# Kernel optimization log

Measured on AMD Instinct MI355X. Metric: run time of the kernel, lower is better.

Reference implementation:

```python
import jax, jax.numpy as jnp
import numpy as np

N = 50000   # nodes
E = 800000  # directed edges
D = 128     # input_feat_dim
H = 128     # hidden1
L = 3       # GatedGraphConv layers
G = 64      # num graphs in batch
NEG_SLOPE = 0.01


def setup_inputs() -> dict:
    key = jax.random.key(0)
    ks = jax.random.split(key, 12)
    s = 1.0 / np.sqrt(H)
    x = jax.random.normal(ks[0], (N, D), jnp.float32)
    edge_index = jax.random.randint(ks[1], (2, E), 0, N)
    batch = jnp.sort(jax.random.randint(ks[2], (N,), 0, G))
    W_gcn = jax.random.normal(ks[3], (D, H), jnp.float32) * s
    b_gcn = jnp.zeros((H,), jnp.float32)
    W_gg = jax.random.normal(ks[4], (L, H, H), jnp.float32) * s   # GatedGraphConv per-layer weight
    W_ih = jax.random.normal(ks[5], (3 * H, H), jnp.float32) * s  # GRUCell input weights (r,z,n)
    W_hh = jax.random.normal(ks[6], (3 * H, H), jnp.float32) * s  # GRUCell hidden weights
    b_ih = jnp.zeros((3 * H,), jnp.float32)
    b_hh = jnp.zeros((3 * H,), jnp.float32)
    W1 = jax.random.normal(ks[7], (H, H), jnp.float32) * s
    b1 = jnp.zeros((H,), jnp.float32)
    W2 = jax.random.normal(ks[8], (H, 1), jnp.float32) * s
    b2 = jnp.zeros((1,), jnp.float32)
    return dict(x=x, edge_index=edge_index, batch=batch, W_gcn=W_gcn, b_gcn=b_gcn,
                W_gg=W_gg, W_ih=W_ih, W_hh=W_hh, b_ih=b_ih, b_hh=b_hh,
                W1=W1, b1=b1, W2=W2, b2=b2)


def _seg(vals, idx, num):
    return jax.ops.segment_sum(vals, idx, num_segments=num)


def _gcn(x, row, col, W, b):
    # PyG GCNConv: add self loops, symmetric norm, aggregate at target (col)
    xw = x @ W
    deg = _seg(jnp.ones((E,), xw.dtype), col, N) + 1.0  # +1 for self loop
    dinv = jax.lax.rsqrt(deg)
    norm = dinv[row] * dinv[col]                         # [E]
    out = _seg(xw[row] * norm[:, None], col, N)          # gather-scale-scatter
    out = out + xw * (dinv * dinv)[:, None]              # self-loop term
    return out + b


def _gru(m, h, W_ih, W_hh, b_ih, b_hh):
    gi = m @ W_ih.T + b_ih
    gh = h @ W_hh.T + b_hh
    ir, iz, inn = jnp.split(gi, 3, axis=-1)
    hr, hz, hn = jnp.split(gh, 3, axis=-1)
    r = jax.nn.sigmoid(ir + hr)
    z = jax.nn.sigmoid(iz + hz)
    n = jnp.tanh(inn + r * hn)
    return (1.0 - z) * n + z * h


def reference(x, edge_index, batch, W_gcn, b_gcn, W_gg, W_ih, W_hh, b_ih, b_hh, W1, b1, W2, b2):
    row, col = edge_index[0], edge_index[1]
    h = jax.nn.leaky_relu(_gcn(x, row, col, W_gcn, b_gcn), NEG_SLOPE)   # [N,H]
    g = h
    for l in range(L):  # GatedGraphConv: message = x_j @ W_l, sum-aggregate at col, GRU update
        m = _seg((g @ W_gg[l])[row], col, N)
        g = _gru(m, g, W_ih, W_hh, b_ih, b_hh)
    h = jax.nn.leaky_relu(g, NEG_SLOPE) + h
    h = jax.nn.leaky_relu(h @ W1 + b1, NEG_SLOPE)
    probs = jax.nn.sigmoid(h @ W2 + b2)                                  # [N,1]
    # maxcut loss: per-graph expected cut
    degrees = _seg(jnp.ones((E,), probs.dtype), row, N)[:, None]         # degree(row) per node
    expected_weight = _seg(probs[row] * probs[col], batch[row], G)       # [G,1]
    expected_degree = _seg(probs * degrees, batch, G)                    # [G,1]
    return -(expected_degree - expected_weight) / 2.0                    # [G,1]
```

## Files before the change

kernel.cpp:

```cpp
#include <hip/hip_runtime.h>
#include <math.h>

#define HD 128
#define NEG 0.01f
#define GD 64
#define LDST 136
#define FST 132

typedef short bf16x8 __attribute__((ext_vector_type(8)));
typedef float floatx4 __attribute__((ext_vector_type(4)));

__device__ __forceinline__ unsigned short f2bf(float f) {
    unsigned int u = __float_as_uint(f);
    u += 0x7fffu + ((u >> 16) & 1u);
    return (unsigned short)(u >> 16);
}
__device__ __forceinline__ float bf2f(unsigned short b) {
    return __uint_as_float(((unsigned int)b) << 16);
}
__device__ __forceinline__ float sigm(float v) { return 1.f / (1.f + __expf(-v)); }

__device__ __forceinline__ void mm64(const unsigned short* __restrict__ ap,
                                     const unsigned short* __restrict__ W,
                                     int m16, int quad, floatx4* acc) {
    #pragma unroll
    for (int ks = 0; ks < 4; ks++) {
        const int koff = ks * 32 + quad * 8;
        bf16x8 a = *(const bf16x8*)(ap + koff);
        #pragma unroll
        for (int cg = 0; cg < 8; cg++) {
            bf16x8 b = *(const bf16x8*)(W + (size_t)(cg * 16 + m16) * HD + koff);
            acc[cg] = __builtin_amdgcn_mfma_f32_16x16x32_bf16(a, b, acc[cg], 0, 0, 0);
        }
    }
}

__device__ __forceinline__ void loadB(const unsigned short* __restrict__ W,
                                      int w, int m16, int quad, bf16x8 bf[2][4]) {
    #pragma unroll
    for (int cgl = 0; cgl < 2; cgl++)
        #pragma unroll
        for (int ks = 0; ks < 4; ks++)
            bf[cgl][ks] = *(const bf16x8*)(W + (size_t)((2 * w + cgl) * 16 + m16) * HD
                                           + ks * 32 + quad * 8);
}
__device__ __forceinline__ void mmAcc32(const unsigned short* __restrict__ Atile,
                                        int m16, int quad, const bf16x8 bf[2][4],
                                        floatx4 acc[2][2]) {
    #pragma unroll
    for (int rg = 0; rg < 2; rg++)
        #pragma unroll
        for (int ks = 0; ks < 4; ks++) {
            bf16x8 a = *(const bf16x8*)(Atile + (rg * 16 + m16) * LDST + ks * 32 + quad * 8);
            acc[rg][0] = __builtin_amdgcn_mfma_f32_16x16x32_bf16(a, bf[0][ks], acc[rg][0], 0, 0, 0);
            acc[rg][1] = __builtin_amdgcn_mfma_f32_16x16x32_bf16(a, bf[1][ks], acc[rg][1], 0, 0, 0);
        }
}

__global__ __launch_bounds__(256) void gemm_mfma(
    const unsigned short* __restrict__ A, const unsigned short* __restrict__ BT,
    float* __restrict__ C32, unsigned short* __restrict__ C16, int M)
{
    __shared__ unsigned short As[128 * LDST];
    __shared__ unsigned short Bs[128 * LDST];
    const int tid = threadIdx.x;
    const int r0 = blockIdx.x * 128;
    {
        int rowi = tid >> 1, half = tid & 1;
        int gr = r0 + rowi; if (gr >= M) gr = M - 1;
        const float4* sa = (const float4*)(A + (size_t)gr * HD + half * 64);
        float4* da = (float4*)(As + rowi * LDST + half * 64);
        const float4* sb = (const float4*)(BT + (size_t)rowi * HD + half * 64);
        float4* db = (float4*)(Bs + rowi * LDST + half * 64);
        #pragma unroll
        for (int i = 0; i < 8; i++) { da[i] = sa[i]; db[i] = sb[i]; }
    }
    __syncthreads();
    const int wave = tid >> 6, lane = tid & 63;
    const int m16 = lane & 15, quad = lane >> 4;
    floatx4 acc[2][8];
    #pragma unroll
    for (int i = 0; i < 2; i++)
        #pragma unroll
        for (int j = 0; j < 8; j++) acc[i][j] = (floatx4){0.f, 0.f, 0.f, 0.f};
    const unsigned short* ar0 = As + (wave * 32 + m16) * LDST;
    const unsigned short* ar1 = As + (wave * 32 + 16 + m16) * LDST;
    #pragma unroll
    for (int ks = 0; ks < 4; ks++) {
        const int koff = ks * 32 + quad * 8;
        bf16x8 a0 = *(const bf16x8*)(ar0 + koff);
        bf16x8 a1 = *(const bf16x8*)(ar1 + koff);
        #pragma unroll
        for (int cg = 0; cg < 8; cg++) {
            bf16x8 b = *(const bf16x8*)(Bs + (cg * 16 + m16) * LDST + koff);
            acc[0][cg] = __builtin_amdgcn_mfma_f32_16x16x32_bf16(a0, b, acc[0][cg], 0, 0, 0);
            acc[1][cg] = __builtin_amdgcn_mfma_f32_16x16x32_bf16(a1, b, acc[1][cg], 0, 0, 0);
        }
    }
    if (C32) {
        #pragma unroll
        for (int rg = 0; rg < 2; rg++)
            #pragma unroll
            for (int cg = 0; cg < 8; cg++)
                #pragma unroll
                for (int i = 0; i < 4; i++) {
                    int r = r0 + wave * 32 + rg * 16 + quad * 4 + i;
                    if (r < M) C32[(size_t)r * HD + cg * 16 + m16] = acc[rg][cg][i];
                }
    }
    __syncthreads();
    #pragma unroll
    for (int rg = 0; rg < 2; rg++)
        #pragma unroll
        for (int cg = 0; cg < 8; cg++)
            #pragma unroll
            for (int i = 0; i < 4; i++)
                As[(wave * 32 + rg * 16 + quad * 4 + i) * LDST + cg * 16 + m16] =
                    f2bf(acc[rg][cg][i]);
    __syncthreads();
    #pragma unroll
    for (int it = 0; it < 8; it++) {
        int idx = it * 2048 + tid * 8;
        int rowi = idx >> 7, c = idx & 127;
        int gr = r0 + rowi;
        if (gr < M) {
            uint4 v = *(const uint4*)(As + rowi * LDST + c);
            *(uint4*)(C16 + (size_t)gr * HD + c) = v;
        }
    }
}

__global__ __launch_bounds__(256) void k_gather_gcn(
    const unsigned short* __restrict__ src, const float* __restrict__ xw,
    const int* __restrict__ csr, const int* __restrict__ offs,
    const float* __restrict__ dinv, const float* __restrict__ bias,
    float* __restrict__ h, unsigned short* __restrict__ g16, int N)
{
    int node = blockIdx.x * 4 + (threadIdx.x >> 6);
    if (node >= N) return;
    int lane = threadIdx.x & 63;
    int s = offs[node], e = offs[node + 1];
    float ax = 0.f, ay = 0.f;
    int j = s;
    for (; j + 4 <= e; j += 4) {
        int r0 = csr[j], r1 = csr[j + 1], r2 = csr[j + 2], r3 = csr[j + 3];
        unsigned int u0 = *(const unsigned int*)(src + (size_t)r0 * HD + lane * 2);
        unsigned int u1 = *(const unsigned int*)(src + (size_t)r1 * HD + lane * 2);
        unsigned int u2 = *(const unsigned int*)(src + (size_t)r2 * HD + lane * 2);
        unsigned int u3 = *(const unsigned int*)(src + (size_t)r3 * HD + lane * 2);
        float s0 = dinv[r0], s1 = dinv[r1], s2 = dinv[r2], s3 = dinv[r3];
        ax += __uint_as_float(u0 << 16) * s0 + __uint_as_float(u1 << 16) * s1
            + __uint_as_float(u2 << 16) * s2 + __uint_as_float(u3 << 16) * s3;
        ay += __uint_as_float(u0 & 0xffff0000u) * s0 + __uint_as_float(u1 & 0xffff0000u) * s1
            + __uint_as_float(u2 & 0xffff0000u) * s2 + __uint_as_float(u3 & 0xffff0000u) * s3;
    }
    for (; j < e; j++) {
        int r = csr[j];
        unsigned int u = *(const unsigned int*)(src + (size_t)r * HD + lane * 2);
        float sc = dinv[r];
        ax += __uint_as_float(u << 16) * sc;
        ay += __uint_as_float(u & 0xffff0000u) * sc;
    }
    float dn = dinv[node];
    float dv2 = dn * dn;
    size_t i = (size_t)node * HD + lane * 2;
    float v0 = ax * dn + xw[i] * dv2 + bias[lane * 2];
    float v1 = ay * dn + xw[i + 1] * dv2 + bias[lane * 2 + 1];
    v0 = v0 > 0.f ? v0 : v0 * NEG;
    v1 = v1 > 0.f ? v1 : v1 * NEG;
    h[i] = v0; h[i + 1] = v1;
    *(unsigned int*)(g16 + i) = (unsigned int)f2bf(v0) | ((unsigned int)f2bf(v1) << 16);
}

__global__ __launch_bounds__(256) void k_gather_m(
    const unsigned short* __restrict__ src, const int* __restrict__ csr,
    const int* __restrict__ offs, unsigned short* __restrict__ out16, int N)
{
    int node = blockIdx.x * 4 + (threadIdx.x >> 6);
    if (node >= N) return;
    int lane = threadIdx.x & 63;
    int s = offs[node], e = offs[node + 1];
    float ax = 0.f, ay = 0.f;
    int j = s;
    for (; j + 4 <= e; j += 4) {
        int r0 = csr[j], r1 = csr[j + 1], r2 = csr[j + 2], r3 = csr[j + 3];
        unsigned int u0 = *(const unsigned int*)(src + (size_t)r0 * HD + lane * 2);
        unsigned int u1 = *(const unsigned int*)(src + (size_t)r1 * HD + lane * 2);
        unsigned int u2 = *(const unsigned int*)(src + (size_t)r2 * HD + lane * 2);
        unsigned int u3 = *(const unsigned int*)(src + (size_t)r3 * HD + lane * 2);
        ax += __uint_as_float(u0 << 16) + __uint_as_float(u1 << 16)
            + __uint_as_float(u2 << 16) + __uint_as_float(u3 << 16);
        ay += __uint_as_float(u0 & 0xffff0000u) + __uint_as_float(u1 & 0xffff0000u)
            + __uint_as_float(u2 & 0xffff0000u) + __uint_as_float(u3 & 0xffff0000u);
    }
    for (; j < e; j++) {
        int r = csr[j];
        unsigned int u = *(const unsigned int*)(src + (size_t)r * HD + lane * 2);
        ax += __uint_as_float(u << 16);
        ay += __uint_as_float(u & 0xffff0000u);
    }
    unsigned int p = (unsigned int)f2bf(ax) | ((unsigned int)f2bf(ay) << 16);
    *(unsigned int*)(out16 + (size_t)node * HD + lane * 2) = p;
}

__global__ __launch_bounds__(256, 5) void k_gru_gates(
    const unsigned short* __restrict__ m_bf, const unsigned short* __restrict__ g_bf,
    const unsigned short* __restrict__ Wih, const unsigned short* __restrict__ Whh,
    const float* __restrict__ b_ih, const float* __restrict__ b_hh,
    unsigned short* __restrict__ g16_out, int M)
{
    __shared__ unsigned short sh[2 * 32 * LDST];
    unsigned short* Am = sh;
    unsigned short* Ag = sh + 32 * LDST;
    const int tid = threadIdx.x;
    const int r0 = blockIdx.x * 32;
    #pragma unroll
    for (int it = 0; it < 2; it++) {
        int idx = it * 2048 + tid * 8;
        int rowi = idx >> 7, c = idx & 127;
        int gr = r0 + rowi; if (gr >= M) gr = M - 1;
        *(float4*)(Am + rowi * LDST + c) = *(const float4*)(m_bf + (size_t)gr * HD + c);
        *(float4*)(Ag + rowi * LDST + c) = *(const float4*)(g_bf + (size_t)gr * HD + c);
    }
    __syncthreads();
    const int w = tid >> 6, l = tid & 63;
    const int m16 = l & 15, quad = l >> 4;

    floatx4 accA[2][2], accB[2][2];
    bf16x8 bf[2][4];
    #pragma unroll
    for (int rg = 0; rg < 2; rg++)
        #pragma unroll
        for (int c = 0; c < 2; c++) {
            accA[rg][c] = (floatx4){0.f, 0.f, 0.f, 0.f};
            accB[rg][c] = (floatx4){0.f, 0.f, 0.f, 0.f};
        }
    loadB(Wih, w, m16, quad, bf);
    mmAcc32(Am, m16, quad, bf, accA);
    loadB(Whh, w, m16, quad, bf);
    mmAcc32(Ag, m16, quad, bf, accA);
    loadB(Whh + 256 * HD, w, m16, quad, bf);
    mmAcc32(Ag, m16, quad, bf, accB);
    #pragma unroll
    for (int cgl = 0; cgl < 2; cgl++) {
        int c = (2 * w + cgl) * 16 + m16;
        float br = b_ih[c] + b_hh[c];
        float bhn = b_hh[256 + c];
        #pragma unroll
        for (int rg = 0; rg < 2; rg++)
            #pragma unroll
            for (int i = 0; i < 4; i++) {
                float r = sigm(accA[rg][cgl][i] + br);
                accB[rg][cgl][i] = r * (accB[rg][cgl][i] + bhn);
            }
    }
    loadB(Wih + 256 * HD, w, m16, quad, bf);
    mmAcc32(Am, m16, quad, bf, accB);
    #pragma unroll
    for (int rg = 0; rg < 2; rg++)
        #pragma unroll
        for (int c = 0; c < 2; c++) accA[rg][c] = (floatx4){0.f, 0.f, 0.f, 0.f};
    loadB(Wih + 128 * HD, w, m16, quad, bf);
    mmAcc32(Am, m16, quad, bf, accA);
    loadB(Whh + 128 * HD, w, m16, quad, bf);
    mmAcc32(Ag, m16, quad, bf, accA);
    float ov[2][2][4];
    #pragma unroll
    for (int cgl = 0; cgl < 2; cgl++) {
        int c = (2 * w + cgl) * 16 + m16;
        float bz = b_ih[128 + c] + b_hh[128 + c];
        float bin = b_ih[256 + c];
        #pragma unroll
        for (int rg = 0; rg < 2; rg++)
            #pragma unroll
            for (int i = 0; i < 4; i++) {
                float z = sigm(accA[rg][cgl][i] + bz);
                float n = tanhf(accB[rg][cgl][i] + bin);
                float gv = bf2f(Ag[(rg * 16 + quad * 4 + i) * LDST + c]);
                ov[cgl][rg][i] = (1.f - z) * n + z * gv;
            }
    }
    __syncthreads();
    float* shf = (float*)sh;
    #pragma unroll
    for (int cgl = 0; cgl < 2; cgl++) {
        int c = (2 * w + cgl) * 16 + m16;
        #pragma unroll
        for (int rg = 0; rg < 2; rg++)
            #pragma unroll
            for (int i = 0; i < 4; i++)
                shf[(rg * 16 + quad * 4 + i) * FST + c] = ov[cgl][rg][i];
    }
    __syncthreads();
    #pragma unroll
    for (int it = 0; it < 2; it++) {
        int idx = it * 2048 + tid * 8;
        int rowi = idx >> 7, c = idx & 127;
        int gr = r0 + rowi;
        if (gr < M) {
            float4 v0 = *(const float4*)(shf + rowi * FST + c);
            float4 v1 = *(const float4*)(shf + rowi * FST + c + 4);
            uint4 st;
            st.x = (unsigned int)f2bf(v0.x) | ((unsigned int)f2bf(v0.y) << 16);
            st.y = (unsigned int)f2bf(v0.z) | ((unsigned int)f2bf(v0.w) << 16);
            st.z = (unsigned int)f2bf(v1.x) | ((unsigned int)f2bf(v1.y) << 16);
            st.w = (unsigned int)f2bf(v1.z) | ((unsigned int)f2bf(v1.w) << 16);
            *(uint4*)(g16_out + (size_t)gr * HD + c) = st;
        }
    }
}

__global__ __launch_bounds__(256, 4) void k_head_fused(
    const unsigned short* __restrict__ g_bf, const float* __restrict__ h,
    const unsigned short* __restrict__ W1T, const float* __restrict__ b1,
    const float* __restrict__ W2, const float* __restrict__ b2,
    float* __restrict__ probs, int M)
{
    __shared__ unsigned short As[64 * LDST];
    const int tid = threadIdx.x;
    const int r0 = blockIdx.x * 64;
    {
        int rowi = tid >> 2, q = tid & 3;
        int gr = r0 + rowi; if (gr >= M) gr = M - 1;
        const unsigned short* gp = g_bf + (size_t)gr * HD + q * 32;
        const float* hp = h + (size_t)gr * HD + q * 32;
        unsigned short* dst = As + rowi * LDST + q * 32;
        #pragma unroll
        for (int i = 0; i < 32; i += 4) {
            ushort4 gu = *(const ushort4*)(gp + i);
            float4 hv = *(const float4*)(hp + i);
            ushort4 o;
            float v;
            v = bf2f(gu.x); v = v > 0.f ? v : v * NEG; o.x = f2bf(v + hv.x);
            v = bf2f(gu.y); v = v > 0.f ? v : v * NEG; o.y = f2bf(v + hv.y);
            v = bf2f(gu.z); v = v > 0.f ? v : v * NEG; o.z = f2bf(v + hv.z);
            v = bf2f(gu.w); v = v > 0.f ? v : v * NEG; o.w = f2bf(v + hv.w);
            *(ushort4*)(dst + i) = o;
        }
    }
    __syncthreads();
    const int w = tid >> 6, l = tid & 63;
    const int m16 = l & 15, quad = l >> 4;
    floatx4 acc[8];
    #pragma unroll
    for (int j = 0; j < 8; j++) acc[j] = (floatx4){0.f, 0.f, 0.f, 0.f};
    mm64(As + (w * 16 + m16) * LDST, W1T, m16, quad, acc);
    #pragma unroll
    for (int i = 0; i < 4; i++) {
        float s = 0.f;
        #pragma unroll
        for (int cg = 0; cg < 8; cg++) {
            int c = cg * 16 + m16;
            float v = acc[cg][i] + b1[c];
            v = v > 0.f ? v : v * NEG;
            s += v * W2[c];
        }
        s += __shfl_xor(s, 1); s += __shfl_xor(s, 2);
        s += __shfl_xor(s, 4); s += __shfl_xor(s, 8);
        int r = r0 + w * 16 + quad * 4 + i;
        if (m16 == 0 && r < M) probs[r] = sigm(s + b2[0]);
    }
}

__global__ void k_prep_w(const float* __restrict__ W_gcn, const float* __restrict__ W_gg,
                         const float* __restrict__ W_ih, const float* __restrict__ W_hh,
                         const float* __restrict__ W1, unsigned short* __restrict__ Wq) {
    int i = blockIdx.x * blockDim.x + threadIdx.x;
    if (i >= 180224) return;
    float v;
    if (i < 16384) {
        int n = i >> 7, k = i & 127;
        v = W_gcn[k * 128 + n];
    } else if (i < 65536) {
        int j = i - 16384;
        int l = j >> 14, rr = j & 16383;
        int n = rr >> 7, k = rr & 127;
        v = W_gg[l * 16384 + k * 128 + n];
    } else if (i < 114688) {
        v = W_ih[i - 65536];
    } else if (i < 163840) {
        v = W_hh[i - 114688];
    } else {
        int j = i - 163840;
        int n = j >> 7, k = j & 127;
        v = W1[k * 128 + n];
    }
    Wq[i] = f2bf(v);
}

__global__ void k_cast_x(const float* __restrict__ s, unsigned short* __restrict__ d, int n2) {
    int i = blockIdx.x * blockDim.x + threadIdx.x;
    if (i >= n2) return;
    float2 v = *(const float2*)(s + (size_t)i * 2);
    unsigned int p = (unsigned int)f2bf(v.x) | ((unsigned int)f2bf(v.y) << 16);
    *(unsigned int*)(d + (size_t)i * 2) = p;
}

__global__ void k_hist(const int* __restrict__ col, int* __restrict__ cnt4,
                       int* __restrict__ rank, int N, int E) {
    int e = blockIdx.x * blockDim.x + threadIdx.x;
    if (e < E) {
        int s = blockIdx.x & 3;
        rank[e] = atomicAdd(&cnt4[s * N + col[e]], 1);
    }
}

#define SCHUNK 2048
__global__ __launch_bounds__(256) void k_scan1(const int* __restrict__ cnt4,
                                               int* __restrict__ excl,
                                               int* __restrict__ bsum, int N) {
    __shared__ int ts[256];
    int t = threadIdx.x;
    int base = blockIdx.x * SCHUNK + t * 8;
    int v[8]; int s = 0;
    #pragma unroll
    for (int q = 0; q < 8; q++) {
        int i = base + q;
        v[q] = (i < N) ? (cnt4[i] + cnt4[N + i] + cnt4[2 * N + i] + cnt4[3 * N + i]) : 0;
        s += v[q];
    }
    ts[t] = s;
    __syncthreads();
    for (int off = 1; off < 256; off <<= 1) {
        int a = (t >= off) ? ts[t - off] : 0;
        __syncthreads();
        ts[t] += a;
        __syncthreads();
    }
    int run = ts[t] - s;
    #pragma unroll
    for (int q = 0; q < 8; q++) { int i = base + q; if (i < N) excl[i] = run; run += v[q]; }
    if (t == 255) bsum[blockIdx.x] = ts[255];
}

__global__ void k_scan2(int* bsum, int nb) {
    if (threadIdx.x == 0) {
        int run = 0;
        for (int b = 0; b < nb; b++) { int v = bsum[b]; bsum[b] = run; run += v; }
    }
}

__global__ void k_csrfin(const int* __restrict__ excl, const int* __restrict__ bsum,
                         const int* __restrict__ cnt4, int* __restrict__ offs,
                         int* __restrict__ sbase, float* __restrict__ dinv, int N, int E) {
    int i = blockIdx.x * blockDim.x + threadIdx.x;
    if (i >= N) return;
    int o = excl[i] + bsum[i >> 11];
    offs[i] = o;
    if (i == 0) offs[N] = E;
    int c0 = cnt4[i], c1 = cnt4[N + i], c2 = cnt4[2 * N + i], c3 = cnt4[3 * N + i];
    sbase[i] = o;
    sbase[N + i] = o + c0;
    sbase[2 * N + i] = o + c0 + c1;
    sbase[3 * N + i] = o + c0 + c1 + c2;
    dinv[i] = rsqrtf((float)(c0 + c1 + c2 + c3) + 1.f);
}

__global__ void k_fill(const int* __restrict__ row, const int* __restrict__ col,
                       const int* __restrict__ sbase, const int* __restrict__ rank,
                       int* __restrict__ csr_rows, int N, int E) {
    int e = blockIdx.x * blockDim.x + threadIdx.x;
    if (e >= E) return;
    int s = (e >> 8) & 3;
    csr_rows[sbase[s * N + col[e]] + rank[e]] = row[e];
}

__global__ __launch_bounds__(256) void k_loss_edge(const float* __restrict__ probs,
                                                   const int* __restrict__ row,
                                                   const int* __restrict__ col,
                                                   const int* __restrict__ batch,
                                                   float* __restrict__ ed,
                                                   float* __restrict__ ew, int E) {
    __shared__ float bd[GD], be[GD];
    if (threadIdx.x < GD) { bd[threadIdx.x] = 0.f; be[threadIdx.x] = 0.f; }
    __syncthreads();
    for (int e = blockIdx.x * blockDim.x + threadIdx.x; e < E; e += gridDim.x * blockDim.x) {
        int r = row[e];
        float pr = probs[r];
        int b = batch[r];
        atomicAdd(&bd[b], pr);
        atomicAdd(&be[b], pr * probs[col[e]]);
    }
    __syncthreads();
    if (threadIdx.x < GD) {
        atomicAdd(&ed[threadIdx.x], bd[threadIdx.x]);
        atomicAdd(&ew[threadIdx.x], be[threadIdx.x]);
    }
}

__global__ void k_finalize(const float* __restrict__ ed, const float* __restrict__ ew,
                           float* __restrict__ out) {
    int g = threadIdx.x;
    if (g < GD) out[g] = -(ed[g] - ew[g]) * 0.5f;
}

extern "C" void kernel_launch(void* const* d_in, const int* in_sizes, int n_in,
                              void* d_out, int out_size, void* d_ws, size_t ws_size,
                              hipStream_t stream) {
    const float* x     = (const float*)d_in[0];
    const int*   ei    = (const int*)d_in[1];
    const int*   batch = (const int*)d_in[2];
    const float* W_gcn = (const float*)d_in[3];
    const float* b_gcn = (const float*)d_in[4];
    const float* W_gg  = (const float*)d_in[5];
    const float* W_ih  = (const float*)d_in[6];
    const float* W_hh  = (const float*)d_in[7];
    const float* b_ih  = (const float*)d_in[8];
    const float* b_hh  = (const float*)d_in[9];
    const float* W1    = (const float*)d_in[10];
    const float* b1    = (const float*)d_in[11];
    const float* W2    = (const float*)d_in[12];
    const float* b2    = (const float*)d_in[13];
    float* out = (float*)d_out;

    const int N = in_sizes[2];
    const int E = in_sizes[1] / 2;
    const int* row = ei;
    const int* col = ei + E;
    const size_t NH = (size_t)N * HD;

    float* F = (float*)d_ws;
    float* f_h  = F + 0 * NH;
    float* f_xw = F + 1 * NH;
    unsigned short* U = (unsigned short*)(F + 2 * NH);
    unsigned short* x_bf  = U;
    unsigned short* g_bf  = U + 1 * NH;
    unsigned short* t_bf  = U + 2 * NH;
    unsigned short* m_bf  = U + 3 * NH;
    unsigned short* Wq    = U + 4 * NH;
    unsigned short* WgcnT = Wq;
    unsigned short* WggT  = Wq + 16384;
    unsigned short* Wih16 = Wq + 65536;
    unsigned short* Whh16 = Wq + 114688;
    unsigned short* W1T   = Wq + 163840;
    float* S = (float*)(Wq + 180224);
    float* f_dinv  = S;
    float* f_probs = S + N;
    float* f_ed    = S + 2 * N;
    float* f_ew    = f_ed + GD;
    int* I = (int*)(f_ew + GD);
    int* i_cnt4  = I;
    int* i_excl  = I + 4 * N;
    int* i_offs  = I + 5 * N;
    int* i_bsum  = I + 6 * N + 8;
    int* i_sbase = I + 6 * N + 128;
    int* i_rank  = I + 10 * N + 128;
    int* i_csr   = i_rank + E;

    const int nb_scan = (N + SCHUNK - 1) / SCHUNK;
    const int gb32 = (N + 31) / 32;
    const int gb64 = (N + 63) / 64;
    const int gb128 = (N + 127) / 128;
    const int eg = (E + 255) / 256;
    const int ng = (N + 255) / 256;
    const int gather_grid = (N + 3) / 4;

    hipMemsetAsync(i_cnt4, 0, sizeof(int) * 4 * (size_t)N, stream);
    hipMemsetAsync(f_ed, 0, sizeof(float) * 2 * GD, stream);

    k_prep_w<<<704, 256, 0, stream>>>(W_gcn, W_gg, W_ih, W_hh, W1, Wq);
    k_cast_x<<<(int)((NH / 2 + 255) / 256), 256, 0, stream>>>(x, x_bf, (int)(NH / 2));

    k_hist<<<eg, 256, 0, stream>>>(col, i_cnt4, i_rank, N, E);
    k_scan1<<<nb_scan, 256, 0, stream>>>(i_cnt4, i_excl, i_bsum, N);
    k_scan2<<<1, 64, 0, stream>>>(i_bsum, nb_scan);
    k_csrfin<<<ng, 256, 0, stream>>>(i_excl, i_bsum, i_cnt4, i_offs, i_sbase, f_dinv, N, E);
    k_fill<<<eg, 256, 0, stream>>>(row, col, i_sbase, i_rank, i_csr, N, E);

    gemm_mfma<<<gb128, 256, 0, stream>>>(x_bf, WgcnT, f_xw, t_bf, N);
    k_gather_gcn<<<gather_grid, 256, 0, stream>>>(t_bf, f_xw, i_csr, i_offs, f_dinv,
                                                  b_gcn, f_h, g_bf, N);

    for (int l = 0; l < 3; l++) {
        gemm_mfma<<<gb128, 256, 0, stream>>>(g_bf, WggT + (size_t)l * 16384,
                                             nullptr, t_bf, N);
        k_gather_m<<<gather_grid, 256, 0, stream>>>(t_bf, i_csr, i_offs, m_bf, N);
        k_gru_gates<<<gb32, 256, 0, stream>>>(m_bf, g_bf, Wih16, Whh16, b_ih, b_hh,
                                              g_bf, N);
    }

    k_head_fused<<<gb64, 256, 0, stream>>>(g_bf, f_h, W1T, b1, W2, b2, f_probs, N);

    k_loss_edge<<<1024, 256, 0, stream>>>(f_probs, row, col, batch, f_ed, f_ew, E);
    k_finalize<<<1, 64, 0, stream>>>(f_ed, f_ew, out);
}
```

Baseline: 610.8 us.

## Split wavefront into four edge groups with 16-byte row loads in gathers

The GCN and message gather kernels now split each 64-lane wavefront into four 16-lane subgroups. Each subgroup handles a different neighbor edge and loads 8 bf16 values per lane as one 16-byte vector, instead of the whole wave reading one 4-byte slice per edge. Partial sums are combined with cross-lane shuffles, and one subgroup writes the result with vector stores. This is meant to raise memory-level parallelism and cut load instructions in the latency-bound gather, at the cost of shuffle reductions and idle lanes on low-degree tails. The GRU gate kernel's launch-bounds occupancy hint also goes from 5 to 6.

```diff
diff --git a/kernel.cpp b/kernel.cpp
--- a/kernel.cpp
+++ b/kernel.cpp
@@ -139,37 +139,56 @@
     int node = blockIdx.x * 4 + (threadIdx.x >> 6);
     if (node >= N) return;
     int lane = threadIdx.x & 63;
+    int sub = lane >> 4, cl = lane & 15;
     int s = offs[node], e = offs[node + 1];
-    float ax = 0.f, ay = 0.f;
+    float acc[8] = {0.f, 0.f, 0.f, 0.f, 0.f, 0.f, 0.f, 0.f};
     int j = s;
-    for (; j + 4 <= e; j += 4) {
-        int r0 = csr[j], r1 = csr[j + 1], r2 = csr[j + 2], r3 = csr[j + 3];
-        unsigned int u0 = *(const unsigned int*)(src + (size_t)r0 * HD + lane * 2);
-        unsigned int u1 = *(const unsigned int*)(src + (size_t)r1 * HD + lane * 2);
-        unsigned int u2 = *(const unsigned int*)(src + (size_t)r2 * HD + lane * 2);
-        unsigned int u3 = *(const unsigned int*)(src + (size_t)r3 * HD + lane * 2);
-        float s0 = dinv[r0], s1 = dinv[r1], s2 = dinv[r2], s3 = dinv[r3];
-        ax += __uint_as_float(u0 << 16) * s0 + __uint_as_float(u1 << 16) * s1
-            + __uint_as_float(u2 << 16) * s2 + __uint_as_float(u3 << 16) * s3;
-        ay += __uint_as_float(u0 & 0xffff0000u) * s0 + __uint_as_float(u1 & 0xffff0000u) * s1
-            + __uint_as_float(u2 & 0xffff0000u) * s2 + __uint_as_float(u3 & 0xffff0000u) * s3;
-    }
-    for (; j < e; j++) {
-        int r = csr[j];
-        unsigned int u = *(const unsigned int*)(src + (size_t)r * HD + lane * 2);
-        float sc = dinv[r];
-        ax += __uint_as_float(u << 16) * sc;
-        ay += __uint_as_float(u & 0xffff0000u) * sc;
-    }
-    float dn = dinv[node];
-    float dv2 = dn * dn;
-    size_t i = (size_t)node * HD + lane * 2;
-    float v0 = ax * dn + xw[i] * dv2 + bias[lane * 2];
-    float v1 = ay * dn + xw[i + 1] * dv2 + bias[lane * 2 + 1];
-    v0 = v0 > 0.f ? v0 : v0 * NEG;
-    v1 = v1 > 0.f ? v1 : v1 * NEG;
-    h[i] = v0; h[i + 1] = v1;
-    *(unsigned int*)(g16 + i) = (unsigned int)f2bf(v0) | ((unsigned int)f2bf(v1) << 16);
+    for (; j + 8 <= e; j += 8) {
+        int ra = csr[j + sub], rb = csr[j + 4 + sub];
+        float sa = dinv[ra], sb = dinv[rb];
+        bf16x8 va = *(const bf16x8*)(src + (size_t)ra * HD + cl * 8);
+        bf16x8 vb = *(const bf16x8*)(src + (size_t)rb * HD + cl * 8);
+        #pragma unroll
+        for (int q = 0; q < 8; q++)
+            acc[q] += bf2f((unsigned short)va[q]) * sa + bf2f((unsigned short)vb[q]) * sb;
+    }
+    for (; j < e; j += 4) {
+        int jj = j + sub;
+        if (jj < e) {
+            int r = csr[jj];
+            float sc = dinv[r];
+            bf16x8 v = *(const bf16x8*)(src + (size_t)r * HD + cl * 8);
+            #pragma unroll
+            for (int q = 0; q < 8; q++)
+                acc[q] += bf2f((unsigned short)v[q]) * sc;
+        }
+    }
+    #pragma unroll
+    for (int q = 0; q < 8; q++) {
+        acc[q] += __shfl_xor(acc[q], 16);
+        acc[q] += __shfl_xor(acc[q], 32);
+    }
+    if (sub == 0) {
+        float dn = dinv[node], dv2 = dn * dn;
+        size_t base = (size_t)node * HD + cl * 8;
+        float4 xv0 = *(const float4*)(xw + base);
+        float4 xv1 = *(const float4*)(xw + base + 4);
+        float xs[8] = {xv0.x, xv0.y, xv0.z, xv0.w, xv1.x, xv1.y, xv1.z, xv1.w};
+        float o[8];
+        #pragma unroll
+        for (int q = 0; q < 8; q++) {
+            float v = acc[q] * dn + xs[q] * dv2 + bias[cl * 8 + q];
+            o[q] = v > 0.f ? v : v * NEG;
+        }
+        *(float4*)(h + base) = (float4){o[0], o[1], o[2], o[3]};
+        *(float4*)(h + base + 4) = (float4){o[4], o[5], o[6], o[7]};
+        uint4 st;
+        st.x = (unsigned int)f2bf(o[0]) | ((unsigned int)f2bf(o[1]) << 16);
+        st.y = (unsigned int)f2bf(o[2]) | ((unsigned int)f2bf(o[3]) << 16);
+        st.z = (unsigned int)f2bf(o[4]) | ((unsigned int)f2bf(o[5]) << 16);
+        st.w = (unsigned int)f2bf(o[6]) | ((unsigned int)f2bf(o[7]) << 16);
+        *(uint4*)(g16 + base) = st;
+    }
 }
 
 __global__ __launch_bounds__(256) void k_gather_m(
@@ -179,31 +198,44 @@
     int node = blockIdx.x * 4 + (threadIdx.x >> 6);
     if (node >= N) return;
     int lane = threadIdx.x & 63;
+    int sub = lane >> 4, cl = lane & 15;
     int s = offs[node], e = offs[node + 1];
-    float ax = 0.f, ay = 0.f;
+    float acc[8] = {0.f, 0.f, 0.f, 0.f, 0.f, 0.f, 0.f, 0.f};
     int j = s;
-    for (; j + 4 <= e; j += 4) {
-        int r0 = csr[j], r1 = csr[j + 1], r2 = csr[j + 2], r3 = csr[j + 3];
-        unsigned int u0 = *(const unsigned int*)(src + (size_t)r0 * HD + lane * 2);
-        unsigned int u1 = *(const unsigned int*)(src + (size_t)r1 * HD + lane * 2);
-        unsigned int u2 = *(const unsigned int*)(src + (size_t)r2 * HD + lane * 2);
-        unsigned int u3 = *(const unsigned int*)(src + (size_t)r3 * HD + lane * 2);
-        ax += __uint_as_float(u0 << 16) + __uint_as_float(u1 << 16)
-            + __uint_as_float(u2 << 16) + __uint_as_float(u3 << 16);
-        ay += __uint_as_float(u0 & 0xffff0000u) + __uint_as_float(u1 & 0xffff0000u)
-            + __uint_as_float(u2 & 0xffff0000u) + __uint_as_float(u3 & 0xffff0000u);
-    }
-    for (; j < e; j++) {
-        int r = csr[j];
-        unsigned int u = *(const unsigned int*)(src + (size_t)r * HD + lane * 2);
-        ax += __uint_as_float(u << 16);
-        ay += __uint_as_float(u & 0xffff0000u);
-    }
-    unsigned int p = (unsigned int)f2bf(ax) | ((unsigned int)f2bf(ay) << 16);
-    *(unsigned int*)(out16 + (size_t)node * HD + lane * 2) = p;
-}
-
-__global__ __launch_bounds__(256, 5) void k_gru_gates(
+    for (; j + 8 <= e; j += 8) {
+        int ra = csr[j + sub], rb = csr[j + 4 + sub];
+        bf16x8 va = *(const bf16x8*)(src + (size_t)ra * HD + cl * 8);
+        bf16x8 vb = *(const bf16x8*)(src + (size_t)rb * HD + cl * 8);
+        #pragma unroll
+        for (int q = 0; q < 8; q++)
+            acc[q] += bf2f((unsigned short)va[q]) + bf2f((unsigned short)vb[q]);
+    }
+    for (; j < e; j += 4) {
+        int jj = j + sub;
+        if (jj < e) {
+            int r = csr[jj];
+            bf16x8 v = *(const bf16x8*)(src + (size_t)r * HD + cl * 8);
+            #pragma unroll
+            for (int q = 0; q < 8; q++)
+                acc[q] += bf2f((unsigned short)v[q]);
+        }
+    }
+    #pragma unroll
+    for (int q = 0; q < 8; q++) {
+        acc[q] += __shfl_xor(acc[q], 16);
+        acc[q] += __shfl_xor(acc[q], 32);
+    }
+    if (sub == 0) {
+        uint4 st;
+        st.x = (unsigned int)f2bf(acc[0]) | ((unsigned int)f2bf(acc[1]) << 16);
+        st.y = (unsigned int)f2bf(acc[2]) | ((unsigned int)f2bf(acc[3]) << 16);
+        st.z = (unsigned int)f2bf(acc[4]) | ((unsigned int)f2bf(acc[5]) << 16);
+        st.w = (unsigned int)f2bf(acc[6]) | ((unsigned int)f2bf(acc[7]) << 16);
+        *(uint4*)(out16 + (size_t)node * HD + cl * 8) = st;
+    }
+}
+
+__global__ __launch_bounds__(256, 6) void k_gru_gates(
     const unsigned short* __restrict__ m_bf, const unsigned short* __restrict__ g_bf,
     const unsigned short* __restrict__ Wih, const unsigned short* __restrict__ Whh,
     const float* __restrict__ b_ih, const float* __restrict__ b_hh,
```

New measurement: 633.8 us. +3.8%, slower.
